# Performance work log

Hardware: AMD Instinct MI355X
Metric: run time of the kernel (lower is better)

The kernel has to match this reference:

```python
import jax, jax.numpy as jnp
import numpy as np

TAU = 2.0      # LIF membrane time constant
VTH = 1.0      # spiking threshold (spikingjelly default)
ALPHA = 4.0    # surrogate sigmoid sharpness (spikingjelly Sigmoid default)
EPS = 1e-5     # BatchNorm eps


@jax.custom_vjp
def spike(v):
    # Heaviside(v) with surrogate sigmoid gradient
    return (v >= 0.0).astype(v.dtype)

def _spike_fwd(v):
    return spike(v), v

def _spike_bwd(v, g):
    s = jax.nn.sigmoid(ALPHA * v)
    return (g * ALPHA * s * (1.0 - s),)

spike.defvjp(_spike_fwd, _spike_bwd)


def lif(x_seq):
    # MultiStepLIFNode: x_seq [T, B, C], v_reset=0 (hard reset), detach_reset=True
    def step(v, xt):
        v = v + (xt - v) / TAU           # membrane decay + charge
        s = spike(v - VTH)               # fire
        v = v * (1.0 - jax.lax.stop_gradient(s))  # detached hard reset to 0
        return v, s
    v0 = jnp.zeros_like(x_seq[0])
    _, s_seq = jax.lax.scan(step, v0, x_seq)
    return s_seq


def block(h, w, b, gamma, beta):
    # h: [B, C_in, T] -> conv1d(k=3, pad=1) -> BN (batch stats) -> LIF -> [B, E, T]
    y = jax.lax.conv_general_dilated(h, w, window_strides=(1,), padding=[(1, 1)],
                                     dimension_numbers=('NCH', 'OIH', 'NCH'))
    y = y + b[None, :, None]
    mu = y.mean(axis=(0, 2), keepdims=True)
    var = y.var(axis=(0, 2), keepdims=True)
    y = (y - mu) * jax.lax.rsqrt(var + EPS) * gamma[None, :, None] + beta[None, :, None]
    s = lif(jnp.transpose(y, (2, 0, 1)))        # [T, B, E]
    return jnp.transpose(s, (1, 2, 0))          # [B, E, T]


def setup_inputs() -> dict:
    key = jax.random.key(0)
    ks = jax.random.split(key, 8)
    B, T, Cin, E, O = 64, 1024, 8, 256, 63
    return {
        'x':       jax.random.normal(ks[0], (B, T, Cin), jnp.float32),
        'conv0_w': jax.random.normal(ks[1], (E, Cin, 3), jnp.float32) * (1.0 / np.sqrt(Cin * 3)),
        'conv0_b': jax.random.normal(ks[2], (E,), jnp.float32) * 0.01,
        'convs_w': jax.random.normal(ks[3], (3, E, E, 3), jnp.float32) * (1.0 / np.sqrt(E * 3)),
        'convs_b': jax.random.normal(ks[4], (3, E), jnp.float32) * 0.01,
        'bn_gamma': jnp.ones((4, E), jnp.float32),
        'bn_beta':  jnp.zeros((4, E), jnp.float32),
        'head_w':  jax.random.normal(ks[5], (O, E), jnp.float32) * (1.0 / np.sqrt(E)),
        'head_b':  jnp.zeros((O,), jnp.float32),
    }


def reference(x, conv0_w, conv0_b, convs_w, convs_b, bn_gamma, bn_beta, head_w, head_b):
    h = jnp.transpose(x, (0, 2, 1))  # [B, C, T]
    h = block(h, conv0_w, conv0_b, bn_gamma[0], bn_beta[0])
    for i in range(convs_w.shape[0]):
        h = block(h, convs_w[i], convs_b[i], bn_gamma[i + 1], bn_beta[i + 1])
    h = h.mean(axis=-1)  # AdaptiveAvgPool1d(1) + squeeze -> [B, E]
    return h @ head_w.T + head_b  # [B, O]
```

## Files before the change

### kernel.cpp

```cpp
#include <hip/hip_runtime.h>
#include <hip/hip_bf16.h>
#include <stdint.h>

#define NB 64
#define NT 1024
#define CIN 8
#define NE 256
#define NO 63
#define TPAD 16
#define TROWS (NT + 2*TPAD)
#define LCH 128
#define LWU 48
#define TT 256

using bf16x8 = __attribute__((ext_vector_type(8))) short;
using f32x4  = __attribute__((ext_vector_type(4))) float;


__global__ void conv0_prep(const float* __restrict__ x, const float* __restrict__ w0,
                           const float* __restrict__ b0, float* __restrict__ y,
                           double* __restrict__ acc0,
                           const float* __restrict__ cw, __hip_bfloat16* __restrict__ wfr) {
    int bid = blockIdx.x;
    if (bid >= 512) {
        int F = (bid - 512) * 256 + threadIdx.x;
        int lane = F & 63;
        int xx = F >> 6;
        int cph = xx & 7;  xx >>= 3;
        int e4  = xx & 15; xx >>= 4;
        int s   = xx & 1;  xx >>= 1;
        int k   = xx % 3;
        int l   = xx / 3;
        int e = e4*16 + (lane & 15);
        int cb = cph*32 + (lane >> 4)*8;
        __hip_bfloat16 outv[8];
        #pragma unroll
        for (int j = 0; j < 8; ++j) {
            float w = cw[((size_t)(l*256 + e)*256 + (cb + j))*3 + k];
            __hip_bfloat16 hi = __float2bfloat16(w);
            if (s == 0) outv[j] = hi;
            else        outv[j] = __float2bfloat16(w - __bfloat162float(hi));
        }
        *(uint4*)(wfr + (size_t)F*8) = *(uint4*)outv;
        return;
    }
    int b = bid >> 3, tc = bid & 7;
    int e = threadIdx.x;
    int t0 = tc * 128;
    __shared__ float xs[1040];
    for (int i = threadIdx.x; i < 1040; i += 256) {
        int t = t0 - 1 + (i >> 3); int c = i & 7;
        xs[i] = (t >= 0 && t < NT) ? x[((size_t)b*NT + t)*CIN + c] : 0.0f;
    }
    __syncthreads();
    float w[24];
    #pragma unroll
    for (int j = 0; j < 24; ++j) w[j] = w0[e*24 + j];
    float bias = b0[e];
    float s = 0.0f, qq = 0.0f;
    for (int dt = 0; dt < 128; ++dt) {
        float acc = bias;
        #pragma unroll
        for (int c = 0; c < 8; ++c)
            #pragma unroll
            for (int k = 0; k < 3; ++k)
                acc += xs[(dt + k)*8 + c] * w[c*3 + k];
        y[((size_t)b*NT + t0 + dt)*NE + e] = acc;
        s += acc; qq += acc*acc;
    }
    atomicAdd(&acc0[e],       (double)s);
    atomicAdd(&acc0[256 + e], (double)qq);
}

template<bool WS>
__global__ void lif_kern(const float* __restrict__ y, const double* __restrict__ acc,
                         const float* __restrict__ gamma, const float* __restrict__ beta,
                         __hip_bfloat16* __restrict__ S, float* __restrict__ pool) {
    int c = blockIdx.x, b = blockIdx.y;
    int e = threadIdx.x;
    double sa = acc[e], qa = acc[256 + e];
    double mean = sa * (1.0/65536.0);
    double var  = qa * (1.0/65536.0) - mean*mean;
    float rs  = (float)(1.0 / sqrt(var + 1e-5));
    float mu  = (float)mean;
    float rsg = rs * gamma[e];
    float bet = beta[e];
    const __hip_bfloat16 z   = __float2bfloat16(0.0f);
    const __hip_bfloat16 one = __float2bfloat16(1.0f);
    if (WS) {
        if (c == 0) {
            for (int r = 0; r < TPAD; ++r) S[((size_t)b*TROWS + r)*NE + e] = z;
        }
        if (c == 7) {
            for (int r = 0; r < TPAD; ++r) S[((size_t)b*TROWS + TPAD + NT + r)*NE + e] = z;
        }
    }
    int t0 = c * LCH;
    int tw = t0 - LWU; if (tw < 0) tw = 0;
    const float* yb = y + (size_t)b*NT*NE + e;
    __hip_bfloat16* sb = S + ((size_t)b*TROWS + TPAD)*NE + e;
    float v = 0.0f;
    #pragma unroll 8
    for (int t = tw; t < t0; ++t) {
        float xx = yb[(size_t)t*NE];
        float yn = (xx - mu)*rsg + bet;
        float d  = __fsub_rn(yn, v);
        v = __fadd_rn(v, __fmul_rn(d, 0.5f));
        v = (v >= 1.0f) ? 0.0f : v;
    }
    float cnt = 0.0f;
    #pragma unroll 8
    for (int t = t0; t < t0 + LCH; ++t) {
        float xx = yb[(size_t)t*NE];
        float yn = (xx - mu)*rsg + bet;
        float d  = __fsub_rn(yn, v);
        v = __fadd_rn(v, __fmul_rn(d, 0.5f));
        bool sp = (v >= 1.0f);
        if (WS) sb[(size_t)t*NE] = sp ? one : z;
        else    cnt += sp ? 1.0f : 0.0f;
        v = sp ? 0.0f : v;
    }
    if (!WS) pool[(size_t)(b*8 + c)*256 + e] = cnt;
}

__global__ __launch_bounds__(256, 2) void conv_mfma(
    const __hip_bfloat16* __restrict__ Sp,
    const __hip_bfloat16* __restrict__ Wfr,
    const float* __restrict__ bias,
    float* __restrict__ y,
    double* __restrict__ acc_out)
{
    __shared__ short Bbuf[260*32];
    __shared__ short Abuf[48*512];
    const int tid  = threadIdx.x;
    const int wave = tid >> 6, lane = tid & 63;
    const int n16  = lane & 15, q = lane >> 4;
    const int we = wave & 1, wt = wave >> 1;
    const int tt = blockIdx.x, et = blockIdx.y, b = blockIdx.z;
    const int t0 = tt * TT;

    f32x4 acc[4][8] = {};
    bf16x8 bfr[8];

    const __hip_bfloat16* Sbase = Sp + ((size_t)b*TROWS + (TPAD - 1 + t0)) * NE;

    for (int ph = 0; ph < 8; ++ph) {
        const int c0 = ph * 32;
        __syncthreads();
        for (int idx = tid; idx < 258*4; idx += 256) {
            int r = idx >> 2, sg = idx & 3;
            uint4 d = *(const uint4*)(Sbase + (size_t)r*NE + c0 + sg*8);
            int sgs = sg ^ ((r >> 1) & 3);
            *(uint4*)((char*)Bbuf + r*64 + sgs*16) = d;
        }
        #pragma unroll
        for (int it = 0; it < 12; ++it) {
            int idx = tid + it*256;
            int chunk = idx >> 6, li = idx & 63;
            int ks = chunk >> 3, e4i = chunk & 7;
            const __hip_bfloat16* src = Wfr + ((((size_t)ks*16 + et*8 + e4i)*8 + ph) << 9) + li*8;
            uint4 d = *(const uint4*)src;
            *(uint4*)(Abuf + chunk*512 + li*8) = d;
        }
        __syncthreads();
        #pragma unroll 1
        for (int kk = 0; kk < 3; ++kk) {
            #pragma unroll
            for (int g = 0; g < 8; ++g) {
                int row = wt*128 + g*16 + n16 + kk;
                int sgs = q ^ ((row >> 1) & 3);
                bfr[g] = *(const bf16x8*)((const char*)Bbuf + row*64 + sgs*16);
            }
            #pragma unroll
            for (int s = 0; s < 2; ++s) {
                const short* ab = Abuf + ((kk*2 + s)*8 + we*4)*512 + lane*8;
                bf16x8 afr[4];
                #pragma unroll
                for (int f = 0; f < 4; ++f)
                    afr[f] = *(const bf16x8*)(ab + f*512);
                #pragma unroll
                for (int f = 0; f < 4; ++f)
                    #pragma unroll
                    for (int g = 0; g < 8; ++g)
                        acc[f][g] = __builtin_amdgcn_mfma_f32_16x16x32_bf16(afr[f], bfr[g], acc[f][g], 0, 0, 0);
            }
        }
    }

    float ls[16], lq[16];
    #pragma unroll
    for (int f = 0; f < 4; ++f) {
        int e_loc = et*128 + we*64 + f*16 + q*4;
        float4 bv = *(const float4*)(bias + e_loc);
        float s0=0,s1=0,s2=0,s3=0, q0=0,q1=0,q2=0,q3=0;
        #pragma unroll
        for (int g = 0; g < 8; ++g) {
            int t = t0 + wt*128 + g*16 + n16;
            f32x4 a = acc[f][g];
            float4 o;
            o.x = a[0] + bv.x; o.y = a[1] + bv.y; o.z = a[2] + bv.z; o.w = a[3] + bv.w;
            *(float4*)(y + ((size_t)b*NT + t)*NE + e_loc) = o;
            s0 += o.x; q0 += o.x*o.x;
            s1 += o.y; q1 += o.y*o.y;
            s2 += o.z; q2 += o.z*o.z;
            s3 += o.w; q3 += o.w*o.w;
        }
        ls[f*4+0]=s0; lq[f*4+0]=q0;
        ls[f*4+1]=s1; lq[f*4+1]=q1;
        ls[f*4+2]=s2; lq[f*4+2]=q2;
        ls[f*4+3]=s3; lq[f*4+3]=q3;
    }
    #pragma unroll
    for (int off = 1; off < 16; off <<= 1) {
        #pragma unroll
        for (int i = 0; i < 16; ++i) {
            ls[i] += __shfl_xor(ls[i], off, 64);
            lq[i] += __shfl_xor(lq[i], off, 64);
        }
    }
    __syncthreads();
    float* red = (float*)Bbuf;
    if (n16 == 0 && wt == 0) {
        #pragma unroll
        for (int f = 0; f < 4; ++f)
            #pragma unroll
            for (int r = 0; r < 4; ++r) {
                int el = we*64 + f*16 + q*4 + r;
                red[el] = ls[f*4+r]; red[128+el] = lq[f*4+r];
            }
    }
    __syncthreads();
    if (n16 == 0 && wt == 1) {
        #pragma unroll
        for (int f = 0; f < 4; ++f)
            #pragma unroll
            for (int r = 0; r < 4; ++r) {
                int el = we*64 + f*16 + q*4 + r;
                red[el] += ls[f*4+r]; red[128+el] += lq[f*4+r];
            }
    }
    __syncthreads();
    if (tid < 128) {
        int e = et*128 + tid;
        atomicAdd(&acc_out[e],       (double)red[tid]);
        atomicAdd(&acc_out[256 + e], (double)red[128 + tid]);
    }
}

__global__ void head_final(const float* __restrict__ pool, const float* __restrict__ hw,
                           const float* __restrict__ hb, float* __restrict__ out) {
    int b = blockIdx.x;
    int tid = threadIdx.x;
    __shared__ float pooled[256];
    float s = 0.0f;
    #pragma unroll
    for (int c = 0; c < 8; ++c) s += pool[(size_t)(b*8 + c)*256 + tid];
    pooled[tid] = s * (1.0f/1024.0f);
    __syncthreads();
    if (tid < NO) {
        float acc = hb[tid];
        for (int c = 0; c < 256; ++c) acc += pooled[c] * hw[tid*256 + c];
        out[b*NO + tid] = acc;
    }
}

extern "C" void kernel_launch(void* const* d_in, const int* in_sizes, int n_in,
                              void* d_out, int out_size, void* d_ws, size_t ws_size,
                              hipStream_t stream) {
    (void)in_sizes; (void)n_in; (void)out_size; (void)ws_size;
    const float* x       = (const float*)d_in[0];
    const float* conv0_w = (const float*)d_in[1];
    const float* conv0_b = (const float*)d_in[2];
    const float* convs_w = (const float*)d_in[3];
    const float* convs_b = (const float*)d_in[4];
    const float* bn_g    = (const float*)d_in[5];
    const float* bn_b    = (const float*)d_in[6];
    const float* head_w  = (const float*)d_in[7];
    const float* head_b  = (const float*)d_in[8];
    float* out = (float*)d_out;

    char* ws = (char*)d_ws;
    float*          y    = (float*)ws;
    __hip_bfloat16* S    = (__hip_bfloat16*)(ws + 67108864);
    __hip_bfloat16* Wfr  = (__hip_bfloat16*)(ws + 101711872);
    double*         acc  = (double*)(ws + 104071168);
    float*          pool = (float*)(ws + 104087552);

    conv0_prep<<<1088, 256, 0, stream>>>(x, conv0_w, conv0_b, y, acc, convs_w, Wfr);
    lif_kern<true><<<dim3(8, 64), 256, 0, stream>>>(y, acc, bn_g, bn_b, S, nullptr);

    for (int l = 0; l < 3; ++l) {
        conv_mfma<<<dim3(4, 2, 64), 256, 0, stream>>>(S, Wfr + (size_t)l*393216,
                                                      convs_b + l*256, y, acc + (l+1)*512);
        const float* g = bn_g + (l+1)*256;
        const float* bb = bn_b + (l+1)*256;
        if (l < 2) lif_kern<true ><<<dim3(8, 64), 256, 0, stream>>>(y, acc + (l+1)*512, g, bb, S, nullptr);
        else       lif_kern<false><<<dim3(8, 64), 256, 0, stream>>>(y, acc + (l+1)*512, g, bb, S, pool);
    }
    head_final<<<64, 256, 0, stream>>>(pool, head_w, head_b, out);
}
```

Before: 338.1 us.

## Fuse all stages into one cooperative persistent kernel with grid syncs

Merges weight prep, conv0, the LIF stages, the MFMA convs and the head into a single cooperative kernel of 512 blocks, separated by grid-wide syncs, with a multi-kernel fallback if the cooperative launch fails. The aim is to remove per-kernel launch gaps and tail drain between the nine dependent stages. Each block now uses a larger shared-memory allocation for every stage, and the weight split is spread over all blocks. Grid syncs cost something, and if occupancy of 2 blocks per CU cannot be met the launch fails and falls back.

```diff
diff --git a/kernel.cpp b/kernel.cpp
--- a/kernel.cpp
+++ b/kernel.cpp
@@ -1,4 +1,5 @@
 #include <hip/hip_runtime.h>
+#include <hip/hip_cooperative_groups.h>
 #include <hip/hip_bf16.h>
 #include <stdint.h>
 
@@ -12,18 +13,19 @@
 #define LCH 128
 #define LWU 48
 #define TT 256
+#define SMEM_BYTES 65792
+
+namespace cg = cooperative_groups;
 
 using bf16x8 = __attribute__((ext_vector_type(8))) short;
 using f32x4  = __attribute__((ext_vector_type(4))) float;
 
 
-__global__ void conv0_prep(const float* __restrict__ x, const float* __restrict__ w0,
-                           const float* __restrict__ b0, float* __restrict__ y,
-                           double* __restrict__ acc0,
-                           const float* __restrict__ cw, __hip_bfloat16* __restrict__ wfr) {
-    int bid = blockIdx.x;
-    if (bid >= 512) {
-        int F = (bid - 512) * 256 + threadIdx.x;
+
+__device__ __forceinline__ void prep_w_dev(const float* __restrict__ cw,
+                                           __hip_bfloat16* __restrict__ wfr, int bid) {
+    for (int it = threadIdx.x; it < 288; it += 256) {
+        int F = bid*288 + it;
         int lane = F & 63;
         int xx = F >> 6;
         int cph = xx & 7;  xx >>= 3;
@@ -42,12 +44,15 @@
             else        outv[j] = __float2bfloat16(w - __bfloat162float(hi));
         }
         *(uint4*)(wfr + (size_t)F*8) = *(uint4*)outv;
-        return;
-    }
+    }
+}
+
+__device__ __forceinline__ void conv0_dev(const float* __restrict__ x, const float* __restrict__ w0,
+                                          const float* __restrict__ b0, float* __restrict__ y,
+                                          double* __restrict__ acc0, float* xs, int bid) {
     int b = bid >> 3, tc = bid & 7;
     int e = threadIdx.x;
     int t0 = tc * 128;
-    __shared__ float xs[1040];
     for (int i = threadIdx.x; i < 1040; i += 256) {
         int t = t0 - 1 + (i >> 3); int c = i & 7;
         xs[i] = (t >= 0 && t < NT) ? x[((size_t)b*NT + t)*CIN + c] : 0.0f;
@@ -73,10 +78,10 @@
 }
 
 template<bool WS>
-__global__ void lif_kern(const float* __restrict__ y, const double* __restrict__ acc,
-                         const float* __restrict__ gamma, const float* __restrict__ beta,
-                         __hip_bfloat16* __restrict__ S, float* __restrict__ pool) {
-    int c = blockIdx.x, b = blockIdx.y;
+__device__ __forceinline__ void lif_dev(const float* __restrict__ y, const double* __restrict__ acc,
+                                        const float* __restrict__ gamma, const float* __restrict__ beta,
+                                        __hip_bfloat16* __restrict__ S, float* __restrict__ pool, int bid) {
+    int c = bid & 7, b = bid >> 3;
     int e = threadIdx.x;
     double sa = acc[e], qa = acc[256 + e];
     double mean = sa * (1.0/65536.0);
@@ -123,20 +128,19 @@
     if (!WS) pool[(size_t)(b*8 + c)*256 + e] = cnt;
 }
 
-__global__ __launch_bounds__(256, 2) void conv_mfma(
-    const __hip_bfloat16* __restrict__ Sp,
-    const __hip_bfloat16* __restrict__ Wfr,
-    const float* __restrict__ bias,
-    float* __restrict__ y,
-    double* __restrict__ acc_out)
-{
-    __shared__ short Bbuf[260*32];
-    __shared__ short Abuf[48*512];
+__device__ __forceinline__ void conv_dev(const __hip_bfloat16* __restrict__ Sp,
+                                         const __hip_bfloat16* __restrict__ Wfr,
+                                         const float* __restrict__ bias,
+                                         float* __restrict__ y,
+                                         double* __restrict__ acc_out,
+                                         char* smem, int bid) {
+    short* Bbuf = (short*)smem;
+    short* Abuf = (short*)(smem + 16640);
     const int tid  = threadIdx.x;
     const int wave = tid >> 6, lane = tid & 63;
     const int n16  = lane & 15, q = lane >> 4;
     const int we = wave & 1, wt = wave >> 1;
-    const int tt = blockIdx.x, et = blockIdx.y, b = blockIdx.z;
+    const int tt = bid & 3, et = (bid >> 2) & 1, b = bid >> 3;
     const int t0 = tt * TT;
 
     f32x4 acc[4][8] = {};
@@ -247,11 +251,10 @@
     }
 }
 
-__global__ void head_final(const float* __restrict__ pool, const float* __restrict__ hw,
-                           const float* __restrict__ hb, float* __restrict__ out) {
-    int b = blockIdx.x;
+__device__ __forceinline__ void head_dev(const float* __restrict__ pool, const float* __restrict__ hw,
+                                         const float* __restrict__ hb, float* __restrict__ out,
+                                         float* pooled, int b) {
     int tid = threadIdx.x;
-    __shared__ float pooled[256];
     float s = 0.0f;
     #pragma unroll
     for (int c = 0; c < 8; ++c) s += pool[(size_t)(b*8 + c)*256 + tid];
@@ -262,6 +265,56 @@
         for (int c = 0; c < 256; ++c) acc += pooled[c] * hw[tid*256 + c];
         out[b*NO + tid] = acc;
     }
+}
+
+__global__ __launch_bounds__(256, 2) void mega(
+    const float* __restrict__ x, const float* __restrict__ conv0_w, const float* __restrict__ conv0_b,
+    const float* __restrict__ convs_w, const float* __restrict__ convs_b,
+    const float* __restrict__ bn_g, const float* __restrict__ bn_b,
+    const float* __restrict__ head_w, const float* __restrict__ head_b,
+    float* __restrict__ y, __hip_bfloat16* __restrict__ S, __hip_bfloat16* __restrict__ Wfr,
+    double* __restrict__ acc, float* __restrict__ pool, float* __restrict__ out)
+{
+    cg::grid_group grid = cg::this_grid();
+    __shared__ __align__(16) char smem[SMEM_BYTES];
+    const int bid = blockIdx.x;
+
+    prep_w_dev(convs_w, Wfr, bid);
+    conv0_dev(x, conv0_w, conv0_b, y, acc, (float*)smem, bid);
+    grid.sync();
+    lif_dev<true>(y, acc, bn_g, bn_b, S, nullptr, bid);
+    grid.sync();
+    #pragma unroll 1
+    for (int l = 0; l < 3; ++l) {
+        conv_dev(S, Wfr + (size_t)l*393216, convs_b + l*256, y, acc + (size_t)(l+1)*512, smem, bid);
+        grid.sync();
+        if (l < 2) lif_dev<true >(y, acc + (size_t)(l+1)*512, bn_g + (l+1)*256, bn_b + (l+1)*256, S, nullptr, bid);
+        else       lif_dev<false>(y, acc + (size_t)(l+1)*512, bn_g + (l+1)*256, bn_b + (l+1)*256, S, pool, bid);
+        grid.sync();
+    }
+    if (bid < 64) head_dev(pool, head_w, head_b, out, (float*)smem, bid);
+}
+
+__global__ __launch_bounds__(256, 2) void k_p0(const float* x, const float* w0, const float* b0,
+                                               float* y, double* acc0,
+                                               const float* cw, __hip_bfloat16* wfr) {
+    __shared__ float xs[1040];
+    prep_w_dev(cw, wfr, blockIdx.x);
+    conv0_dev(x, w0, b0, y, acc0, xs, blockIdx.x);
+}
+template<bool WS>
+__global__ void k_lif(const float* y, const double* acc, const float* g, const float* bb,
+                      __hip_bfloat16* S, float* pool) {
+    lif_dev<WS>(y, acc, g, bb, S, pool, blockIdx.x);
+}
+__global__ __launch_bounds__(256, 2) void k_conv(const __hip_bfloat16* Sp, const __hip_bfloat16* Wfr,
+                                                 const float* bias, float* y, double* acc_out) {
+    __shared__ __align__(16) char smem[SMEM_BYTES];
+    conv_dev(Sp, Wfr, bias, y, acc_out, smem, blockIdx.x);
+}
+__global__ void k_head(const float* pool, const float* hw, const float* hb, float* out) {
+    __shared__ float pooled[256];
+    head_dev(pool, hw, hb, out, pooled, blockIdx.x);
 }
 
 extern "C" void kernel_launch(void* const* d_in, const int* in_sizes, int n_in,
@@ -286,16 +339,23 @@
     double*         acc  = (double*)(ws + 104071168);
     float*          pool = (float*)(ws + 104087552);
 
-    conv0_prep<<<1088, 256, 0, stream>>>(x, conv0_w, conv0_b, y, acc, convs_w, Wfr);
-    lif_kern<true><<<dim3(8, 64), 256, 0, stream>>>(y, acc, bn_g, bn_b, S, nullptr);
-
-    for (int l = 0; l < 3; ++l) {
-        conv_mfma<<<dim3(4, 2, 64), 256, 0, stream>>>(S, Wfr + (size_t)l*393216,
-                                                      convs_b + l*256, y, acc + (l+1)*512);
-        const float* g = bn_g + (l+1)*256;
-        const float* bb = bn_b + (l+1)*256;
-        if (l < 2) lif_kern<true ><<<dim3(8, 64), 256, 0, stream>>>(y, acc + (l+1)*512, g, bb, S, nullptr);
-        else       lif_kern<false><<<dim3(8, 64), 256, 0, stream>>>(y, acc + (l+1)*512, g, bb, S, pool);
-    }
-    head_final<<<64, 256, 0, stream>>>(pool, head_w, head_b, out);
-}
+    void* kargs[] = { (void*)&x, (void*)&conv0_w, (void*)&conv0_b, (void*)&convs_w, (void*)&convs_b,
+                      (void*)&bn_g, (void*)&bn_b, (void*)&head_w, (void*)&head_b,
+                      (void*)&y, (void*)&S, (void*)&Wfr, (void*)&acc, (void*)&pool, (void*)&out };
+    hipError_t err = hipLaunchCooperativeKernel((const void*)mega, dim3(512), dim3(256),
+                                                kargs, 0, stream);
+    if (err != hipSuccess) {
+        (void)hipGetLastError();
+        k_p0<<<512, 256, 0, stream>>>(x, conv0_w, conv0_b, y, acc, convs_w, Wfr);
+        k_lif<true><<<512, 256, 0, stream>>>(y, acc, bn_g, bn_b, S, nullptr);
+        for (int l = 0; l < 3; ++l) {
+            k_conv<<<512, 256, 0, stream>>>(S, Wfr + (size_t)l*393216, convs_b + l*256,
+                                            y, acc + (size_t)(l+1)*512);
+            const float* g  = bn_g + (l+1)*256;
+            const float* bb = bn_b + (l+1)*256;
+            if (l < 2) k_lif<true ><<<512, 256, 0, stream>>>(y, acc + (size_t)(l+1)*512, g, bb, S, nullptr);
+            else       k_lif<false><<<512, 256, 0, stream>>>(y, acc + (size_t)(l+1)*512, g, bb, S, pool);
+        }
+        k_head<<<64, 256, 0, stream>>>(pool, head_w, head_b, out);
+    }
+}
```

Measured after the change: 897.1 us. 165% more time.
